# Kernel tuning notes

Hardware: AMD Instinct MI355X
Metric: run time of the kernel (lower is better)

Reference implementation:

```python
import jax, jax.numpy as jnp
import numpy as np

E, B, N, F, F1D, H, L, H2, PE_DIM = 4, 16384, 1024, 64, 64, 256, 2, 256, 63
TOPK_MEM = 16      # self.top_K: memory retrieval top-k
W0_SIREN = 30.0    # SIREN omega_0 for 'sine' nonlinearity
NUM_FREQ = 10      # PosEncoding num_frequencies
LINE_DIM = 64      # feat_shapes[0]


def _ln(h, g, b):
    m = jnp.mean(h, axis=-1, keepdims=True)
    v = jnp.mean((h - m) ** 2, axis=-1, keepdims=True)
    return (h - m) / jnp.sqrt(v + 1e-5) * g + b


def _pos_enc(coords):
    # NeRF positional encoding: [coords, sin/cos interleaved per coord per freq]
    freqs = 2.0 ** jnp.arange(NUM_FREQ, dtype=coords.dtype)
    scaled = coords[..., None] * freqs * jnp.pi            # (B, 3, NF)
    sc = jnp.stack([jnp.sin(scaled), jnp.cos(scaled)], axis=-1)  # (B, 3, NF, 2)
    return jnp.concatenate([coords, sc.reshape(coords.shape[0], -1)], axis=-1)  # (B, 63)


def _forward(x, lines, mem_k, mem_v, enc_w0, enc_b0, enc_wh, enc_bh, enc_wo, enc_bo,
             ln_g, ln_b, wq, wk, wv, ad_w0, ad_b0, ad_w1, ad_b1, ad_ln_g, ad_ln_b,
             mg_w0, mg_b0, mg_w1, mg_b1, fw0, fb0, fw1, fb1, fw2, fb2, fw3, fb3, route_k):
    coords = x[:, :3]
    # --- 1D line feature interpolation (param_feats) ---
    p = x[:, 3] * (LINE_DIM - 1)
    pf = jnp.floor(p)
    w = p - pf
    il = pf.astype(jnp.int32)
    ih = jnp.clip(pf + 1.0, 0.0, LINE_DIM - 1).astype(jnp.int32)
    f1d = lines[0][:, il] + w * (lines[0][:, ih] - lines[0][:, il])  # (F1D, B)
    param_feats = f1d.T                                              # (B, F1D)

    pe_x = _pos_enc(coords)                                          # (B, 63)
    scale = float(F) ** 0.5

    def expert(ew0, eb0, ewh, ebh, ewo, ebo, wq_e, wk_e, wv_e, mk, mv,
               aw0, ab0, aw1, ab1, ag, ab):
        # SIREN encoder MLP
        h = jnp.sin(W0_SIREN * (pe_x @ ew0 + eb0))
        for l in range(L):
            h = jnp.sin(W0_SIREN * (h @ ewh[l] + ebh[l]))
        mlp_feats = h @ ewo + ebo                          # (B, F)
        q = _ln(mlp_feats, ln_g, ln_b) @ wq_e              # (B, F)
        kp = mk @ wk_e                                     # (N, F) precomputed keys
        vp = mv @ wv_e                                     # (N, F) precomputed values
        scores = q @ kp.T                                  # (B, N)
        _, idx = jax.lax.top_k(scores, TOPK_MEM)           # (B, K)
        k_top = kp[idx]                                    # (B, K, F)
        v_top = vp[idx]                                    # (B, K, F)
        pfe = jnp.broadcast_to(param_feats[:, None, :], (param_feats.shape[0], TOPK_MEM, F1D))
        a = jnp.concatenate([v_top, pfe], axis=-1)         # (B, K, F+F1D)
        a = jax.nn.relu(a @ aw0 + ab0) @ aw1 + ab1
        adapted = v_top + _ln(a, ag, ab)
        attn = jax.nn.softmax(jnp.einsum('bf,bkf->bk', q, k_top) / scale, axis=-1)
        return jnp.einsum('bk,bkf->bf', attn, adapted) + mlp_feats

    # compute every expert densely (vectorized), then gather routed top-k outputs
    all_out = jax.vmap(expert)(enc_w0, enc_b0, enc_wh, enc_bh, enc_wo, enc_bo,
                               wq, wk, wv, mem_k, mem_v,
                               ad_w0, ad_b0, ad_w1, ad_b1, ad_ln_g, ad_ln_b)  # (E, B, F)

    raw_q = jax.nn.relu(coords @ mg_w0 + mg_b0) @ mg_w1 + mg_b1   # manager_net (B, E)
    probs = jnp.clip(jax.nn.softmax(raw_q, axis=-1), 1e-8, None)
    vals, tidx = jax.lax.top_k(probs, route_k)                    # (B, k)
    vals = vals / jnp.sum(vals, axis=-1, keepdims=True)
    gathered = jnp.take_along_axis(jnp.swapaxes(all_out, 0, 1), tidx[..., None], axis=1)  # (B, k, F)
    spatial = jnp.sum(vals[..., None] * gathered, axis=1)         # (B, F)

    h = jax.nn.relu(spatial @ fw0 + fb0)
    h = jax.nn.relu(h @ fw1 + fb1)
    h = jax.nn.relu(h @ fw2 + fb2)
    refined = jax.nn.sigmoid(h @ fw3 + fb3)
    return refined, raw_q


def setup_inputs() -> dict:
    ks = jax.random.split(jax.random.key(0), 24)
    f32 = jnp.float32
    rn = lambda i, shp, s: jax.random.normal(ks[i], shp, f32) * s
    xav = lambda fi, fo: (2.0 / (fi + fo)) ** 0.5
    return {
        'x': jax.random.uniform(ks[0], (B, 4), f32),
        'lines': jax.random.uniform(ks[1], (1, F1D, LINE_DIM), f32, 0.7, 0.8),
        'mem_k': rn(2, (E, N, F), 1.0),
        'mem_v': rn(3, (E, N, F), 1e-3),
        'enc_w0': rn(4, (E, PE_DIM, H), xav(PE_DIM, H)),
        'enc_b0': jnp.zeros((E, H), f32),
        'enc_wh': rn(5, (E, L, H, H), xav(H, H)),
        'enc_bh': jnp.zeros((E, L, H), f32),
        'enc_wo': rn(6, (E, H, F), xav(H, F)),
        'enc_bo': jnp.zeros((E, F), f32),
        'ln_g': jnp.ones((F,), f32),
        'ln_b': jnp.zeros((F,), f32),
        'wq': rn(7, (E, F, F), xav(F, F)),
        'wk': rn(8, (E, F, F), xav(F, F)),
        'wv': rn(9, (E, F, F), xav(F, F)),
        'ad_w0': rn(10, (E, F + F1D, 64), xav(F + F1D, 64)),
        'ad_b0': rn(11, (E, 64), 1e-3),
        'ad_w1': rn(12, (E, 64, F), xav(64, F)),
        'ad_b1': rn(13, (E, F), 1e-3),
        'ad_ln_g': jnp.ones((E, F), f32),
        'ad_ln_b': jnp.zeros((E, F), f32),
        'mg_w0': rn(14, (3, 64), 0.5),
        'mg_b0': jnp.zeros((64,), f32),
        'mg_w1': rn(15, (64, E), 0.5),
        'mg_b1': jnp.zeros((E,), f32),
        'fw0': rn(16, (F, H2), xav(F, H2)),
        'fb0': rn(17, (H2,), 1e-3),
        'fw1': rn(18, (H2, H2), xav(H2, H2)),
        'fb1': rn(19, (H2,), 1e-3),
        'fw2': rn(20, (H2, H2), xav(H2, H2)),
        'fb2': rn(21, (H2,), 1e-3),
        'fw3': rn(22, (H2, 1), xav(H2, 1)),
        'fb3': rn(23, (1,), 1e-3),
        'route_k': 2,
    }


def reference(x, lines, mem_k, mem_v, enc_w0, enc_b0, enc_wh, enc_bh, enc_wo, enc_bo,
              ln_g, ln_b, wq, wk, wv, ad_w0, ad_b0, ad_w1, ad_b1, ad_ln_g, ad_ln_b,
              mg_w0, mg_b0, mg_w1, mg_b1, fw0, fb0, fw1, fb1, fw2, fb2, fw3, fb3, route_k):
    return _forward(x, lines, mem_k, mem_v, enc_w0, enc_b0, enc_wh, enc_bh, enc_wo, enc_bo,
                    ln_g, ln_b, wq, wk, wv, ad_w0, ad_b0, ad_w1, ad_b1, ad_ln_g, ad_ln_b,
                    mg_w0, mg_b0, mg_w1, mg_b1, fw0, fb0, fw1, fb1, fw2, fb2, fw3, fb3, route_k)
```

## Files before the change

kernel.cpp:

```cpp
#include <hip/hip_runtime.h>
#include <math.h>

#define EE 4
#define BB 16384
#define NN 1024
#define FF 64
#define HH 256
#define PED 63
#define TOPK 16
#define LINE 64
#define TS 32
#define NBX (BB/TS)

#define OFF_KP   0u
#define OFF_VP   262144u
#define OFF_VPA  524288u
#define OFF_PE   786432u
#define OFF_PF   1818624u
#define OFF_EO   2867200u
#define OFF_RW   4964352u
#define OFF_CNT  4997120u
#define OFF_LIST 4997128u
#define OFF_QV   5062664u
#define OFF_SM   7159816u
#define OFF_WP   OFF_EO

__device__ __forceinline__ float wred_sum(float v) {
#pragma unroll
    for (int off = 32; off > 0; off >>= 1) v += __shfl_xor(v, off, 64);
    return v;
}
__device__ __forceinline__ void wred_sum2(float& a, float& b) {
#pragma unroll
    for (int off = 32; off > 0; off >>= 1) {
        a += __shfl_xor(a, off, 64);
        b += __shfl_xor(b, off, 64);
    }
}

__global__ __launch_bounds__(256) void k_prep(
    const float* __restrict__ wv, const float* __restrict__ aw0,
    float* __restrict__ wp)
{
    int e = blockIdx.x;
    __shared__ float sa[FF*FF];
    for (int i = threadIdx.x; i < FF*FF; i += 256)
        sa[i] = aw0[(size_t)e*128*FF + i];
    __syncthreads();
    int f = threadIdx.x & 63, dg = threadIdx.x >> 6;
    for (int d = dg; d < FF; d += 4) {
        const float* wr = wv + (size_t)e*FF*FF + d*FF;
        float a = 0.f;
        for (int c = 0; c < FF; ++c) a = fmaf(wr[c], sa[c*FF+f], a);
        wp[(size_t)e*FF*FF + d*FF + f] = a;
    }
}

__global__ __launch_bounds__(256) void k_proj(
    const float* __restrict__ mem_k, const float* __restrict__ mem_v,
    const float* __restrict__ wk, const float* __restrict__ wv,
    const float* __restrict__ wp,
    float* __restrict__ kp, float* __restrict__ vp, float* __restrict__ vpa)
{
    int e = blockIdx.x >> 6;
    int nbase = (blockIdx.x & 63) * 16;
    __shared__ float swk[FF*FF], swv[FF*FF], swp[FF*FF];
    for (int i = threadIdx.x; i < FF*FF; i += 256) {
        swk[i] = wk[(size_t)e*FF*FF + i];
        swv[i] = wv[(size_t)e*FF*FF + i];
        swp[i] = wp[(size_t)e*FF*FF + i];
    }
    __syncthreads();
    int r4 = threadIdx.x >> 6;
    int f  = threadIdx.x & 63;
#pragma unroll 1
    for (int it = 0; it < 4; ++it) {
        int n = nbase + it*4 + r4;
        const float* mk = mem_k + ((size_t)e*NN + n)*FF;
        const float* mv = mem_v + ((size_t)e*NN + n)*FF;
        float ak = 0.f, av = 0.f, aa = 0.f;
#pragma unroll 1
        for (int c4 = 0; c4 < 16; ++c4) {
            float4 k4 = *(const float4*)&mk[4*c4];
            float4 v4 = *(const float4*)&mv[4*c4];
#pragma unroll
            for (int kk = 0; kk < 4; ++kk) {
                float mkc = (kk==0)?k4.x:((kk==1)?k4.y:((kk==2)?k4.z:k4.w));
                float mvc = (kk==0)?v4.x:((kk==1)?v4.y:((kk==2)?v4.z:v4.w));
                int c = 4*c4 + kk;
                ak = fmaf(mkc, swk[c*FF+f], ak);
                av = fmaf(mvc, swv[c*FF+f], av);
                aa = fmaf(mvc, swp[c*FF+f], aa);
            }
        }
        kp [((size_t)e*NN+n)*FF + f] = ak;
        vp [((size_t)e*NN+n)*FF + f] = av;
        vpa[((size_t)e*NN+n)*FF + f] = aa;
    }
}

__global__ __launch_bounds__(256) void k_route(
    const float* __restrict__ x, const float* __restrict__ lines,
    const float* __restrict__ mg_w0, const float* __restrict__ mg_b0,
    const float* __restrict__ mg_w1, const float* __restrict__ mg_b1,
    float* __restrict__ pe_x, float* __restrict__ pfm,
    float* __restrict__ rawq, float* __restrict__ rw,
    int* __restrict__ counts, int* __restrict__ lists)
{
    __shared__ float slines[LINE*LINE];
    for (int i = threadIdx.x; i < LINE*LINE; i += 256) slines[i] = lines[i];
    __syncthreads();
    int b = blockIdx.x*256 + threadIdx.x;
    float4 xx = ((const float4*)x)[b];
    float c0 = xx.x, c1 = xx.y, c2 = xx.z, c3 = xx.w;

    float p = c3 * (float)(LINE-1);
    float pfl = floorf(p);
    float w = p - pfl;
    int il = (int)pfl;
    int ih = (int)fminf(fmaxf(pfl + 1.f, 0.f), (float)(LINE-1));
    for (int c = 0; c < FF; ++c) {
        float lo = slines[c*LINE+il], hi = slines[c*LINE+ih];
        pfm[(size_t)b*FF + c] = lo + w*(hi-lo);
    }
    float* pe = pe_x + (size_t)b*PED;
    pe[0]=c0; pe[1]=c1; pe[2]=c2;
    const float PI = 3.14159265358979323846f;
    float coords[3] = {c0,c1,c2};
#pragma unroll
    for (int cc = 0; cc < 3; ++cc) {
        float fr = PI;
        for (int k = 0; k < 10; ++k) {
            float s = coords[cc]*fr;
            pe[3 + cc*20 + k*2 + 0] = sinf(s);
            pe[3 + cc*20 + k*2 + 1] = cosf(s);
            fr *= 2.f;
        }
    }
    float acc[4] = {mg_b1[0], mg_b1[1], mg_b1[2], mg_b1[3]};
    for (int j = 0; j < 64; ++j) {
        float h = fmaf(c0, mg_w0[j], fmaf(c1, mg_w0[64+j], fmaf(c2, mg_w0[128+j], mg_b0[j])));
        h = fmaxf(h, 0.f);
#pragma unroll
        for (int e4 = 0; e4 < 4; ++e4) acc[e4] = fmaf(h, mg_w1[j*4+e4], acc[e4]);
    }
#pragma unroll
    for (int e4 = 0; e4 < 4; ++e4) rawq[(size_t)b*4 + e4] = acc[e4];
    float m = fmaxf(fmaxf(acc[0],acc[1]), fmaxf(acc[2],acc[3]));
    float ex[4], den = 0.f;
#pragma unroll
    for (int e4 = 0; e4 < 4; ++e4) { ex[e4] = expf(acc[e4]-m); den += ex[e4]; }
    float pr[4];
#pragma unroll
    for (int e4 = 0; e4 < 4; ++e4) pr[e4] = fmaxf(ex[e4]/den, 1e-8f);
    int i0 = 0;
#pragma unroll
    for (int e4 = 1; e4 < 4; ++e4) if (pr[e4] > pr[i0]) i0 = e4;
    int i1 = -1;
#pragma unroll
    for (int e4 = 0; e4 < 4; ++e4) {
        if (e4 == i0) continue;
        if (i1 < 0 || pr[e4] > pr[i1]) i1 = e4;
    }
    float vs = pr[i0] + pr[i1];
    rw[b*2+0] = pr[i0]/vs;
    rw[b*2+1] = pr[i1]/vs;
    int p0 = atomicAdd(&counts[i0], 1);
    lists[i0*BB + p0] = b*2 + 0;
    int p1 = atomicAdd(&counts[i1], 1);
    lists[i1*BB + p1] = b*2 + 1;
}

__global__ __launch_bounds__(512, 3) void k_mlp(
    const float* __restrict__ pe_x,
    const float* __restrict__ enc_w0, const float* __restrict__ enc_b0,
    const float* __restrict__ enc_wh, const float* __restrict__ enc_bh,
    const float* __restrict__ enc_wo, const float* __restrict__ enc_bo,
    const float* __restrict__ ln_g, const float* __restrict__ ln_b,
    const float* __restrict__ wq,
    const int* __restrict__ counts, const int* __restrict__ lists,
    float* __restrict__ qv, float* __restrict__ smlpw)
{
    const int e = blockIdx.y;
    const int base = blockIdx.x * TS;
    const int cnt = counts[e];
    if (base >= cnt) return;

    __shared__ float sh[TS*HH];
    __shared__ float swt[4096];
    __shared__ int   slist[TS];

    const int tid = threadIdx.x;
    const int lane = tid & 63;
    const int wv = tid >> 6;
    const int r0 = wv*4;

    if (tid < TS) {
        int idx = base + tid;
        if (idx >= cnt) idx = cnt - 1;
        slist[tid] = lists[e*BB + idx];
    }
    __syncthreads();
    for (int i = tid; i < TS*64; i += 512) {
        int s = i >> 6, j = i & 63;
        int bq = slist[s] >> 1;
        sh[s*HH + j] = (j < PED) ? pe_x[(size_t)bq*PED + j] : 0.f;
    }

    float acc[4][4];

    {
        const float* W = enc_w0 + (size_t)e*PED*HH;
#pragma unroll
        for (int s = 0; s < 4; ++s)
#pragma unroll
            for (int j = 0; j < 4; ++j) acc[s][j] = 0.f;
#pragma unroll 1
        for (int t = 0; t < 4; ++t) {
            int rbase = t*16;
            int rows = (PED - rbase < 16) ? (PED - rbase) : 16;
            int total = rows*HH;
            __syncthreads();
            for (int i = tid*4; i < total; i += 2048)
                *(float4*)&swt[i] = *(const float4*)&W[rbase*HH + i];
            __syncthreads();
#pragma unroll 1
            for (int k = 0; k < rows; ++k) {
                float4 w4 = *(const float4*)&swt[k*HH + 4*lane];
#pragma unroll
                for (int s = 0; s < 4; ++s) {
                    float hv = sh[(r0+s)*HH + rbase + k];
                    acc[s][0] = fmaf(hv, w4.x, acc[s][0]);
                    acc[s][1] = fmaf(hv, w4.y, acc[s][1]);
                    acc[s][2] = fmaf(hv, w4.z, acc[s][2]);
                    acc[s][3] = fmaf(hv, w4.w, acc[s][3]);
                }
            }
        }
        __syncthreads();
        float4 b4 = *(const float4*)&enc_b0[e*HH + 4*lane];
#pragma unroll
        for (int s = 0; s < 4; ++s) {
            float4 o;
            o.x = sinf(30.0f*(acc[s][0] + b4.x));
            o.y = sinf(30.0f*(acc[s][1] + b4.y));
            o.z = sinf(30.0f*(acc[s][2] + b4.z));
            o.w = sinf(30.0f*(acc[s][3] + b4.w));
            *(float4*)&sh[(r0+s)*HH + 4*lane] = o;
        }
    }

#pragma unroll 1
    for (int layer = 0; layer < 2; ++layer) {
        const float* W = enc_wh + ((size_t)(e*2+layer))*HH*HH;
#pragma unroll
        for (int s = 0; s < 4; ++s)
#pragma unroll
            for (int j = 0; j < 4; ++j) acc[s][j] = 0.f;
#pragma unroll 1
        for (int t = 0; t < 16; ++t) {
            __syncthreads();
            for (int i = tid*4; i < 4096; i += 2048)
                *(float4*)&swt[i] = *(const float4*)&W[t*16*HH + i];
            __syncthreads();
#pragma unroll 1
            for (int k4 = 0; k4 < 4; ++k4) {
                float4 h4[4];
#pragma unroll
                for (int s = 0; s < 4; ++s)
                    h4[s] = *(const float4*)&sh[(r0+s)*HH + t*16 + 4*k4];
#pragma unroll
                for (int kk = 0; kk < 4; ++kk) {
                    float4 w4 = *(const float4*)&swt[(4*k4+kk)*HH + 4*lane];
#pragma unroll
                    for (int s = 0; s < 4; ++s) {
                        float hv = (kk==0)?h4[s].x:((kk==1)?h4[s].y:((kk==2)?h4[s].z:h4[s].w));
                        acc[s][0] = fmaf(hv, w4.x, acc[s][0]);
                        acc[s][1] = fmaf(hv, w4.y, acc[s][1]);
                        acc[s][2] = fmaf(hv, w4.z, acc[s][2]);
                        acc[s][3] = fmaf(hv, w4.w, acc[s][3]);
                    }
                }
            }
        }
        __syncthreads();
        float4 b4 = *(const float4*)&enc_bh[(e*2+layer)*HH + 4*lane];
#pragma unroll
        for (int s = 0; s < 4; ++s) {
            float4 o;
            o.x = sinf(30.0f*(acc[s][0] + b4.x));
            o.y = sinf(30.0f*(acc[s][1] + b4.y));
            o.z = sinf(30.0f*(acc[s][2] + b4.z));
            o.w = sinf(30.0f*(acc[s][3] + b4.w));
            *(float4*)&sh[(r0+s)*HH + 4*lane] = o;
        }
    }

    float smlp_r[4];
    {
        const float* W = enc_wo + (size_t)e*HH*FF;
        float a2o[4] = {0.f,0.f,0.f,0.f};
#pragma unroll 1
        for (int t = 0; t < 4; ++t) {
            __syncthreads();
            for (int i = tid*4; i < 4096; i += 2048)
                *(float4*)&swt[i] = *(const float4*)&W[t*64*FF + i];
            __syncthreads();
#pragma unroll 1
            for (int k4 = 0; k4 < 16; ++k4) {
                float4 h4[4];
#pragma unroll
                for (int s = 0; s < 4; ++s)
                    h4[s] = *(const float4*)&sh[(r0+s)*HH + t*64 + 4*k4];
#pragma unroll
                for (int kk = 0; kk < 4; ++kk) {
                    float w = swt[(4*k4+kk)*FF + lane];
#pragma unroll
                    for (int s = 0; s < 4; ++s) {
                        float hv = (kk==0)?h4[s].x:((kk==1)?h4[s].y:((kk==2)?h4[s].z:h4[s].w));
                        a2o[s] = fmaf(hv, w, a2o[s]);
                    }
                }
            }
        }
        float bv = enc_bo[e*FF + lane];
#pragma unroll
        for (int s = 0; s < 4; ++s) smlp_r[s] = a2o[s] + bv;
    }

    {
        const float* Wq = wq + (size_t)e*FF*FF;
        __syncthreads();
        for (int i = tid*4; i < 4096; i += 2048)
            *(float4*)&swt[i] = *(const float4*)&Wq[i];
        __syncthreads();
        float g = ln_g[lane], bb2 = ln_b[lane];
#pragma unroll 1
        for (int s = 0; s < 4; ++s) {
            float hv = smlp_r[s];
            float sm = hv, s2 = hv*hv;
            wred_sum2(sm, s2);
            float mean = sm * (1.f/64.f);
            float var = s2 * (1.f/64.f) - mean*mean;
            float lnv = (hv - mean) * rsqrtf(var + 1e-5f) * g + bb2;
            sh[(r0+s)*HH + lane] = lnv;
            float qa = 0.f;
#pragma unroll 1
            for (int c4 = 0; c4 < 16; ++c4) {
                float4 l4 = *(const float4*)&sh[(r0+s)*HH + 4*c4];
                qa = fmaf(l4.x, swt[(4*c4+0)*FF + lane], qa);
                qa = fmaf(l4.y, swt[(4*c4+1)*FF + lane], qa);
                qa = fmaf(l4.z, swt[(4*c4+2)*FF + lane], qa);
                qa = fmaf(l4.w, swt[(4*c4+3)*FF + lane], qa);
            }
            if (base + r0 + s < cnt) {
                size_t entry = (size_t)slist[r0+s];
                qv[entry*FF + lane] = qa;
                smlpw[entry*FF + lane] = smlp_r[s];
            }
        }
    }
}

__global__ __launch_bounds__(512) void k_attn(
    const float* __restrict__ pfm,
    const float* __restrict__ kp, const float* __restrict__ vp,
    const float* __restrict__ vpa,
    const float* __restrict__ qv, const float* __restrict__ smlpw,
    const float* __restrict__ aw0, const float* __restrict__ ab0,
    const float* __restrict__ aw1, const float* __restrict__ ab1,
    const float* __restrict__ adg, const float* __restrict__ adb,
    const int* __restrict__ counts, const int* __restrict__ lists,
    float* __restrict__ eo)
{
    const int e = blockIdx.y;
    const int base = blockIdx.x * TS;
    const int cnt = counts[e];
    if (base >= cnt) return;

    __shared__ float sq[TS*FF];
    __shared__ float su[8192];
    __shared__ float sa0[4096];
    __shared__ float sw1[4096];
    __shared__ int   slist[TS];

    const int tid = threadIdx.x;
    const int lane = tid & 63;
    const int wv = tid >> 6;
    const int r0 = wv*4;

    if (tid < TS) {
        int idx = base + tid;
        if (idx >= cnt) idx = cnt - 1;
        slist[tid] = lists[e*BB + idx];
    }
    __syncthreads();
    {
        int s4 = tid >> 4, c4 = (tid & 15)*4;
        *(float4*)&sq[s4*64 + c4] = *(const float4*)&qv[(size_t)slist[s4]*FF + c4];
        const float* a0bG = aw0 + ((size_t)e*128 + 64)*FF;
        const float* w1G  = aw1 + (size_t)e*FF*FF;
        for (int i = tid*4; i < 4096; i += 2048) {
            *(float4*)&sa0[i] = *(const float4*)&a0bG[i];
            *(float4*)&sw1[i] = *(const float4*)&w1G[i];
        }
    }

    float sc[4][16];
    float* skp = su;
    {
        const float* kpe = kp + (size_t)e*NN*FF;
        const int str = tid >> 3;
        const int stc = (tid & 7) * 8;
#pragma unroll 1
        for (int c = 0; c < 16; ++c) {
            __syncthreads();
            {
                const float* src = kpe + (size_t)(c*64 + str)*FF + stc;
                float* dst = &skp[str*68 + stc];
                *(float4*)(dst+0) = *(const float4*)(src+0);
                *(float4*)(dst+4) = *(const float4*)(src+4);
            }
            __syncthreads();
            float a0 = 0.f, a1 = 0.f, a2s = 0.f, a3 = 0.f;
#pragma unroll
            for (int f4 = 0; f4 < 16; ++f4) {
                float4 k4 = *(const float4*)&skp[lane*68 + 4*f4];
                float4 q0 = *(const float4*)&sq[(r0+0)*64 + 4*f4];
                float4 q1 = *(const float4*)&sq[(r0+1)*64 + 4*f4];
                float4 q2 = *(const float4*)&sq[(r0+2)*64 + 4*f4];
                float4 q3 = *(const float4*)&sq[(r0+3)*64 + 4*f4];
                a0 = fmaf(k4.x,q0.x,fmaf(k4.y,q0.y,fmaf(k4.z,q0.z,fmaf(k4.w,q0.w,a0))));
                a1 = fmaf(k4.x,q1.x,fmaf(k4.y,q1.y,fmaf(k4.z,q1.z,fmaf(k4.w,q1.w,a1))));
                a2s= fmaf(k4.x,q2.x,fmaf(k4.y,q2.y,fmaf(k4.z,q2.z,fmaf(k4.w,q2.w,a2s))));
                a3 = fmaf(k4.x,q3.x,fmaf(k4.y,q3.y,fmaf(k4.z,q3.z,fmaf(k4.w,q3.w,a3))));
            }
            sc[0][c]=a0; sc[1][c]=a1; sc[2][c]=a2s; sc[3][c]=a3;
        }
    }
    __syncthreads();

    const float* vpe  = vp  + (size_t)e*NN*FF;
    const float* vpae = vpa + (size_t)e*NN*FF;
    const float agv = adg[e*FF + lane], abv = adb[e*FF + lane];
    const float ab0v = ab0[e*FF + lane];
    const float ab1v = ab1[e*FF + lane];
    float* plw = &su[wv*1024];

#pragma unroll
    for (int u = 0; u < 4; ++u) {
        int s = r0 + u;
        int entry = slist[s];
        int bq = entry >> 1;

        float pp = ab0v;
        {
            const float* pfr = pfm + (size_t)bq*FF;
#pragma unroll 1
            for (int c4 = 0; c4 < 16; ++c4) {
                float4 p4 = *(const float4*)&pfr[4*c4];
                pp = fmaf(p4.x, sa0[(4*c4+0)*FF + lane], pp);
                pp = fmaf(p4.y, sa0[(4*c4+1)*FF + lane], pp);
                pp = fmaf(p4.z, sa0[(4*c4+2)*FF + lane], pp);
                pp = fmaf(p4.w, sa0[(4*c4+3)*FF + lane], pp);
            }
        }

        float wr_my = 0.f; int rn_my = 0;
        unsigned taken = 0u;
        bool need = true;
        float bv = -1e30f; int bn = 0x7fffffff;
        float v0max = 0.f, wsum = 0.f;
#pragma unroll
        for (int r = 0; r < TOPK; ++r) {
            if (need) {
                bv = -1e30f; bn = 0x7fffffff;
#pragma unroll
                for (int c = 0; c < 16; ++c) {
                    float v = sc[u][c];
                    int n = c*64 + lane;
                    bool ok = !((taken >> c) & 1u);
                    bool better = ok && (v > bv || (v == bv && n < bn));
                    bv = better ? v : bv;
                    bn = better ? n : bn;
                }
                need = false;
            }
            float rv = bv; int rn = bn;
#pragma unroll
            for (int off = 32; off > 0; off >>= 1) {
                float ov = __shfl_xor(rv, off, 64);
                int on = __shfl_xor(rn, off, 64);
                bool better = (ov > rv) || (ov == rv && on < rn);
                rv = better ? ov : rv;
                rn = better ? on : rn;
            }
            if (r == 0) v0max = rv;
            float wr = expf((rv - v0max) * 0.125f);
            wsum += wr;
            if ((rn & 63) == lane) { taken |= 1u << (rn >> 6); need = true; }
            if (lane == r) { wr_my = wr; rn_my = rn; }
        }

        float oaccv = 0.f;
#pragma unroll
        for (int b4i = 0; b4i < 4; ++b4i) {
            float pav4[4];
#pragma unroll
            for (int j = 0; j < 4; ++j) {
                int r = b4i*4 + j;
                int rn_b = __shfl(rn_my, r, 64);
                float wr_b = __shfl(wr_my, r, 64);
                pav4[j] = vpae[(size_t)rn_b*FF + lane];
                float vv = vpe[(size_t)rn_b*FF + lane];
                oaccv = fmaf(wr_b, vv, oaccv);
            }
            int slot = b4i ^ (lane & 3);
            float4 o;
            o.x = fmaxf(pav4[0] + pp, 0.f);
            o.y = fmaxf(pav4[1] + pp, 0.f);
            o.z = fmaxf(pav4[2] + pp, 0.f);
            o.w = fmaxf(pav4[3] + pp, 0.f);
            *(float4*)&plw[lane*16 + slot*4] = o;
        }
        float a2[16];
#pragma unroll
        for (int r = 0; r < 16; ++r) a2[r] = ab1v;
#pragma unroll 1
        for (int j4 = 0; j4 < 16; ++j4) {
            const float* plj = &plw[j4*64];
#pragma unroll
            for (int jj = 0; jj < 4; ++jj) {
                float w = sw1[(4*j4+jj)*FF + lane];
#pragma unroll
                for (int lq = 0; lq < 4; ++lq) {
                    float4 d = *(const float4*)&plj[jj*16 + ((lq ^ jj) * 4)];
                    a2[4*lq+0] = fmaf(d.x, w, a2[4*lq+0]);
                    a2[4*lq+1] = fmaf(d.y, w, a2[4*lq+1]);
                    a2[4*lq+2] = fmaf(d.z, w, a2[4*lq+2]);
                    a2[4*lq+3] = fmaf(d.w, w, a2[4*lq+3]);
                }
            }
        }
        float oln = 0.f;
#pragma unroll
        for (int r = 0; r < TOPK; ++r) {
            float av = a2[r];
            float sm = av, s2 = av*av;
            wred_sum2(sm, s2);
            float mean = sm * (1.f/64.f);
            float var = s2 * (1.f/64.f) - mean*mean;
            float lnv = (av - mean) * rsqrtf(var + 1e-5f) * agv + abv;
            float wr_b = __shfl(wr_my, r, 64);
            oln = fmaf(wr_b, lnv, oln);
        }
        float res = (oaccv + oln) / wsum + smlpw[(size_t)entry*FF + lane];
        if (base + s < cnt) eo[(size_t)entry*FF + lane] = res;
    }
}

__global__ __launch_bounds__(512, 3) void k_final(
    const float* __restrict__ eo, const float* __restrict__ rw,
    const float* __restrict__ fw0, const float* __restrict__ fb0,
    const float* __restrict__ fw1, const float* __restrict__ fb1,
    const float* __restrict__ fw2, const float* __restrict__ fb2,
    const float* __restrict__ fw3, const float* __restrict__ fb3,
    float* __restrict__ refined)
{
    __shared__ float sh[TS*HH];
    __shared__ float swt[4096];
    const int tid = threadIdx.x, lane = tid & 63, wv = tid >> 6;
    const int sbase = blockIdx.x * TS;
    const int r0 = wv*4;
    for (int i = tid; i < TS*64; i += 512) {
        int s = i >> 6, c = i & 63;
        int b = sbase + s;
        sh[s*HH + c] = rw[b*2]*eo[(size_t)(b*2)*FF + c]
                     + rw[b*2+1]*eo[(size_t)(b*2+1)*FF + c];
    }
    float acc[4][4];
    {
#pragma unroll
        for (int s = 0; s < 4; ++s)
#pragma unroll
            for (int j = 0; j < 4; ++j) acc[s][j] = 0.f;
#pragma unroll 1
        for (int t = 0; t < 4; ++t) {
            __syncthreads();
            for (int i = tid*4; i < 4096; i += 2048)
                *(float4*)&swt[i] = *(const float4*)&fw0[t*16*HH + i];
            __syncthreads();
#pragma unroll 1
            for (int k = 0; k < 16; ++k) {
                float4 w4 = *(const float4*)&swt[k*HH + 4*lane];
#pragma unroll
                for (int s = 0; s < 4; ++s) {
                    float hv = sh[(r0+s)*HH + t*16 + k];
                    acc[s][0] = fmaf(hv, w4.x, acc[s][0]);
                    acc[s][1] = fmaf(hv, w4.y, acc[s][1]);
                    acc[s][2] = fmaf(hv, w4.z, acc[s][2]);
                    acc[s][3] = fmaf(hv, w4.w, acc[s][3]);
                }
            }
        }
        __syncthreads();
        float4 b4 = *(const float4*)&fb0[4*lane];
#pragma unroll
        for (int s = 0; s < 4; ++s) {
            float4 o;
            o.x = fmaxf(acc[s][0] + b4.x, 0.f);
            o.y = fmaxf(acc[s][1] + b4.y, 0.f);
            o.z = fmaxf(acc[s][2] + b4.z, 0.f);
            o.w = fmaxf(acc[s][3] + b4.w, 0.f);
            *(float4*)&sh[(r0+s)*HH + 4*lane] = o;
        }
    }
#pragma unroll 1
    for (int layer = 0; layer < 2; ++layer) {
        const float* W  = layer ? fw2 : fw1;
        const float* bi = layer ? fb2 : fb1;
#pragma unroll
        for (int s = 0; s < 4; ++s)
#pragma unroll
            for (int j = 0; j < 4; ++j) acc[s][j] = 0.f;
#pragma unroll 1
        for (int t = 0; t < 16; ++t) {
            __syncthreads();
            for (int i = tid*4; i < 4096; i += 2048)
                *(float4*)&swt[i] = *(const float4*)&W[t*16*HH + i];
            __syncthreads();
#pragma unroll 1
            for (int k4 = 0; k4 < 4; ++k4) {
                float4 h4[4];
#pragma unroll
                for (int s = 0; s < 4; ++s)
                    h4[s] = *(const float4*)&sh[(r0+s)*HH + t*16 + 4*k4];
#pragma unroll
                for (int kk = 0; kk < 4; ++kk) {
                    float4 w4 = *(const float4*)&swt[(4*k4+kk)*HH + 4*lane];
#pragma unroll
                    for (int s = 0; s < 4; ++s) {
                        float hv = (kk==0)?h4[s].x:((kk==1)?h4[s].y:((kk==2)?h4[s].z:h4[s].w));
                        acc[s][0] = fmaf(hv, w4.x, acc[s][0]);
                        acc[s][1] = fmaf(hv, w4.y, acc[s][1]);
                        acc[s][2] = fmaf(hv, w4.z, acc[s][2]);
                        acc[s][3] = fmaf(hv, w4.w, acc[s][3]);
                    }
                }
            }
        }
        __syncthreads();
        float4 b4 = *(const float4*)&bi[4*lane];
#pragma unroll
        for (int s = 0; s < 4; ++s) {
            float4 o;
            o.x = fmaxf(acc[s][0] + b4.x, 0.f);
            o.y = fmaxf(acc[s][1] + b4.y, 0.f);
            o.z = fmaxf(acc[s][2] + b4.z, 0.f);
            o.w = fmaxf(acc[s][3] + b4.w, 0.f);
            *(float4*)&sh[(r0+s)*HH + 4*lane] = o;
        }
    }
    {
        float4 w4 = *(const float4*)&fw3[4*lane];
#pragma unroll 1
        for (int s = 0; s < 4; ++s) {
            float4 h4 = *(const float4*)&sh[(r0+s)*HH + 4*lane];
            float part = h4.x*w4.x + h4.y*w4.y + h4.z*w4.z + h4.w*w4.w;
            float tot = wred_sum(part) + fb3[0];
            float r = 1.f/(1.f + expf(-tot));
            if (lane == 0) refined[sbase + r0 + s] = r;
        }
    }
}

extern "C" void kernel_launch(void* const* d_in, const int* in_sizes, int n_in,
                              void* d_out, int out_size, void* d_ws, size_t ws_size,
                              hipStream_t stream)
{
    const float* x      = (const float*)d_in[0];
    const float* lines  = (const float*)d_in[1];
    const float* mem_k  = (const float*)d_in[2];
    const float* mem_v  = (const float*)d_in[3];
    const float* enc_w0 = (const float*)d_in[4];
    const float* enc_b0 = (const float*)d_in[5];
    const float* enc_wh = (const float*)d_in[6];
    const float* enc_bh = (const float*)d_in[7];
    const float* enc_wo = (const float*)d_in[8];
    const float* enc_bo = (const float*)d_in[9];
    const float* ln_g   = (const float*)d_in[10];
    const float* ln_b   = (const float*)d_in[11];
    const float* wq     = (const float*)d_in[12];
    const float* wk     = (const float*)d_in[13];
    const float* wv_    = (const float*)d_in[14];
    const float* ad_w0  = (const float*)d_in[15];
    const float* ad_b0  = (const float*)d_in[16];
    const float* ad_w1  = (const float*)d_in[17];
    const float* ad_b1  = (const float*)d_in[18];
    const float* ad_g   = (const float*)d_in[19];
    const float* ad_b   = (const float*)d_in[20];
    const float* mg_w0  = (const float*)d_in[21];
    const float* mg_b0  = (const float*)d_in[22];
    const float* mg_w1  = (const float*)d_in[23];
    const float* mg_b1  = (const float*)d_in[24];
    const float* fw0    = (const float*)d_in[25];
    const float* fb0    = (const float*)d_in[26];
    const float* fw1    = (const float*)d_in[27];
    const float* fb1    = (const float*)d_in[28];
    const float* fw2    = (const float*)d_in[29];
    const float* fb2    = (const float*)d_in[30];
    const float* fw3    = (const float*)d_in[31];
    const float* fb3    = (const float*)d_in[32];

    float* out_ref = (float*)d_out;
    float* out_rq  = (float*)d_out + BB;

    float* ws  = (float*)d_ws;
    float* kp  = ws + OFF_KP;
    float* vp  = ws + OFF_VP;
    float* vpa = ws + OFF_VPA;
    float* pe  = ws + OFF_PE;
    float* pfm = ws + OFF_PF;
    float* eo  = ws + OFF_EO;
    float* rw  = ws + OFF_RW;
    float* qvw = ws + OFF_QV;
    float* smw = ws + OFF_SM;
    float* wpw = ws + OFF_WP;
    int*  cnts = (int*)(ws + OFF_CNT);
    int*  lst  = (int*)(ws + OFF_LIST);

    hipMemsetAsync(cnts, 0, EE*sizeof(int), stream);
    k_prep<<<dim3(EE), dim3(256), 0, stream>>>(wv_, ad_w0, wpw);
    k_proj<<<dim3(EE*64), dim3(256), 0, stream>>>(mem_k, mem_v, wk, wv_, wpw, kp, vp, vpa);
    k_route<<<dim3(BB/256), dim3(256), 0, stream>>>(x, lines, mg_w0, mg_b0, mg_w1, mg_b1,
                                                    pe, pfm, out_rq, rw, cnts, lst);
    k_mlp<<<dim3(NBX, EE), dim3(512), 0, stream>>>(pe,
        enc_w0, enc_b0, enc_wh, enc_bh, enc_wo, enc_bo, ln_g, ln_b, wq,
        cnts, lst, qvw, smw);
    k_attn<<<dim3(NBX, EE), dim3(512), 0, stream>>>(pfm, kp, vp, vpa, qvw, smw,
        ad_w0, ad_b0, ad_w1, ad_b1, ad_g, ad_b, cnts, lst, eo);
    k_final<<<dim3(BB/TS), dim3(512), 0, stream>>>(eo, rw, fw0, fb0, fw1, fb1,
                                                   fw2, fb2, fw3, fb3, out_ref);
}
```

Baseline: 1.433 ms.

## Keep queries in registers via readlane and register-prefetch key tiles in attention

Each wave now holds its four query rows in VGPRs, one feature per lane, and broadcasts them with readlane into scalar operands. This removes the shared-memory query buffer and its LDS reads in the score loop. The next 64-key tile is also prefetched from global memory into registers while the current tile is being scored, then written to shared memory after a barrier. This overlaps global load latency with compute, at the cost of extra registers and readlane/scalar traffic.

```diff
diff --git a/kernel.cpp b/kernel.cpp
--- a/kernel.cpp
+++ b/kernel.cpp
@@ -36,6 +36,9 @@
         a += __shfl_xor(a, off, 64);
         b += __shfl_xor(b, off, 64);
     }
+}
+__device__ __forceinline__ float rdlane(float v, int k) {
+    return __int_as_float(__builtin_amdgcn_readlane(__float_as_int(v), k));
 }
 
 __global__ __launch_bounds__(256) void k_prep(
@@ -378,7 +381,6 @@
     const int cnt = counts[e];
     if (base >= cnt) return;
 
-    __shared__ float sq[TS*FF];
     __shared__ float su[8192];
     __shared__ float sa0[4096];
     __shared__ float sw1[4096];
@@ -395,9 +397,13 @@
         slist[tid] = lists[e*BB + idx];
     }
     __syncthreads();
+
+    float qf[4];
+#pragma unroll
+    for (int s = 0; s < 4; ++s)
+        qf[s] = qv[(size_t)slist[r0+s]*FF + lane];
+
     {
-        int s4 = tid >> 4, c4 = (tid & 15)*4;
-        *(float4*)&sq[s4*64 + c4] = *(const float4*)&qv[(size_t)slist[s4]*FF + c4];
         const float* a0bG = aw0 + ((size_t)e*128 + 64)*FF;
         const float* w1G  = aw1 + (size_t)e*FF*FF;
         for (int i = tid*4; i < 4096; i += 2048) {
@@ -412,30 +418,39 @@
         const float* kpe = kp + (size_t)e*NN*FF;
         const int str = tid >> 3;
         const int stc = (tid & 7) * 8;
+        float4 pre0, pre1;
+        pre0 = *(const float4*)&kpe[(size_t)(0*64 + str)*FF + stc];
+        pre1 = *(const float4*)&kpe[(size_t)(0*64 + str)*FF + stc + 4];
+        *(float4*)&skp[str*68 + stc]     = pre0;
+        *(float4*)&skp[str*68 + stc + 4] = pre1;
+        __syncthreads();
 #pragma unroll 1
         for (int c = 0; c < 16; ++c) {
-            __syncthreads();
-            {
-                const float* src = kpe + (size_t)(c*64 + str)*FF + stc;
-                float* dst = &skp[str*68 + stc];
-                *(float4*)(dst+0) = *(const float4*)(src+0);
-                *(float4*)(dst+4) = *(const float4*)(src+4);
-            }
-            __syncthreads();
+            if (c < 15) {
+                pre0 = *(const float4*)&kpe[(size_t)((c+1)*64 + str)*FF + stc];
+                pre1 = *(const float4*)&kpe[(size_t)((c+1)*64 + str)*FF + stc + 4];
+            }
             float a0 = 0.f, a1 = 0.f, a2s = 0.f, a3 = 0.f;
 #pragma unroll
             for (int f4 = 0; f4 < 16; ++f4) {
                 float4 k4 = *(const float4*)&skp[lane*68 + 4*f4];
-                float4 q0 = *(const float4*)&sq[(r0+0)*64 + 4*f4];
-                float4 q1 = *(const float4*)&sq[(r0+1)*64 + 4*f4];
-                float4 q2 = *(const float4*)&sq[(r0+2)*64 + 4*f4];
-                float4 q3 = *(const float4*)&sq[(r0+3)*64 + 4*f4];
-                a0 = fmaf(k4.x,q0.x,fmaf(k4.y,q0.y,fmaf(k4.z,q0.z,fmaf(k4.w,q0.w,a0))));
-                a1 = fmaf(k4.x,q1.x,fmaf(k4.y,q1.y,fmaf(k4.z,q1.z,fmaf(k4.w,q1.w,a1))));
-                a2s= fmaf(k4.x,q2.x,fmaf(k4.y,q2.y,fmaf(k4.z,q2.z,fmaf(k4.w,q2.w,a2s))));
-                a3 = fmaf(k4.x,q3.x,fmaf(k4.y,q3.y,fmaf(k4.z,q3.z,fmaf(k4.w,q3.w,a3))));
+#pragma unroll
+                for (int kk = 0; kk < 4; ++kk) {
+                    int k = 4*f4 + kk;
+                    float kv = (kk==0)?k4.x:((kk==1)?k4.y:((kk==2)?k4.z:k4.w));
+                    a0 = fmaf(rdlane(qf[0], k), kv, a0);
+                    a1 = fmaf(rdlane(qf[1], k), kv, a1);
+                    a2s= fmaf(rdlane(qf[2], k), kv, a2s);
+                    a3 = fmaf(rdlane(qf[3], k), kv, a3);
+                }
             }
             sc[0][c]=a0; sc[1][c]=a1; sc[2][c]=a2s; sc[3][c]=a3;
+            __syncthreads();
+            if (c < 15) {
+                *(float4*)&skp[str*68 + stc]     = pre0;
+                *(float4*)&skp[str*68 + stc + 4] = pre1;
+                __syncthreads();
+            }
         }
     }
     __syncthreads();
```

Result: slower. 1.472 ms (+2.7%).
